# Optimization experiments

Hardware: AMD Instinct MI355X
Metric: run time of the kernel (lower is better)

Reference implementation:

```python
import jax, jax.numpy as jnp
import numpy as np

NX = 64
NY = 64
PATCH_HW = 3          # half-width -> 6x6 patches
P = 2 * PATCH_HW
SIGMA = 0.92
I0 = 1.0 * 1000.0 * 1.0   # eta * N0 * texp


def setup_inputs() -> dict:
    key = jax.random.key(0)
    B, NSPOTS = 8192, 64
    # spot centers uniform over the grid (matches sample(): mu + eps*std + nx/2)
    z = jax.random.uniform(key, (B, 2 * NSPOTS), dtype=jnp.float32,
                           minval=0.0, maxval=float(NX))
    return {"z": z}


def _lam(t, t0, sigma):
    # 0.5 * (erf((t+0.5-t0)/alpha) - erf((t-0.5-t0)/alpha)), alpha = sqrt(2)*sigma
    alpha = jnp.sqrt(jnp.float32(2.0)) * sigma
    return 0.5 * (jax.lax.erf((t + 0.5 - t0) / alpha)
                  - jax.lax.erf((t - 0.5 - t0) / alpha))


def reference(z):
    B = z.shape[0]
    nspots = z.shape[1] // 2
    z = z.reshape(B, 2, nspots)
    x0 = z[:, 0, :]                      # [B, S]
    y0 = z[:, 1, :]                      # [B, S]

    # integer patch origin (torch .round().int() -> round half to even, like jnp.round)
    px = jnp.round(x0).astype(jnp.int32) - PATCH_HW   # [B, S]
    py = jnp.round(y0).astype(jnp.int32) - PATCH_HW
    valid = (px >= 0) & (px < NX - P) & (py >= 0) & (py < NY - P)

    # spot center in patch-local coordinates
    x0p = x0 - px.astype(jnp.float32)    # [B, S]
    y0p = y0 - py.astype(jnp.float32)

    coords = jnp.arange(P, dtype=jnp.float32)                # [P]
    lx = _lam(coords[None, None, :], x0p[..., None], SIGMA)  # [B, S, P]
    ly = _lam(coords[None, None, :], y0p[..., None], SIGMA)  # [B, S, P]
    # outer product: patch[b,s,i,j] = I0 * lx[b,s,i] * ly[b,s,j]  (ij meshgrid)
    patch = I0 * lx[..., :, None] * ly[..., None, :]          # [B, S, P, P]
    patch = jnp.where(valid[..., None, None], patch, 0.0)

    # scatter-add into the [B, NX, NY] grid via flat indices
    pxs = jnp.where(valid, px, 0)
    pys = jnp.where(valid, py, 0)
    rows = pxs[..., None] + jnp.arange(P)                     # [B, S, P]
    cols = pys[..., None] + jnp.arange(P)                     # [B, S, P]
    flat = (jnp.arange(B, dtype=jnp.int32)[:, None, None, None] * (NX * NY)
            + rows[..., :, None] * NY + cols[..., None, :])   # [B, S, P, P]

    mu = jnp.zeros((B * NX * NY,), jnp.float32)
    mu = mu.at[flat.reshape(-1)].add(patch.reshape(-1))
    return mu.reshape(B, 1, NX, NY)
```

## Files before the change

### kernel.cpp

```cpp
#include <hip/hip_runtime.h>


constexpr int NXc = 64;
constexpr int NYc = 64;
constexpr int PATCH_HW = 3;
constexpr int PP = 6;
constexpr float I0c = 1000.0f;
constexpr float INV_ALPHA = 0.76859415f;

__global__ __launch_bounds__(256) void loc_spots_kernel(
        const float* __restrict__ z, float* __restrict__ out) {
    __shared__ float mu[NXc * NYc];
    const int b   = blockIdx.x;
    const int tid = threadIdx.x;

    float4* mu4 = reinterpret_cast<float4*>(mu);
#pragma unroll
    for (int i = 0; i < 4; ++i)
        mu4[tid + i * 256] = make_float4(0.f, 0.f, 0.f, 0.f);
    __syncthreads();

    const int s = tid & 63;
    const int g = tid >> 6;

    const float x0 = z[b * 128 + s];
    const float y0 = z[b * 128 + 64 + s];

    const int px = (int)rintf(x0) - PATCH_HW;
    const int py = (int)rintf(y0) - PATCH_HW;
    const bool valid = (px >= 0) && (px < NXc - PP) && (py >= 0) && (py < NYc - PP);

    if (valid) {
        const float x0p = x0 - (float)px;
        const float y0p = y0 - (float)py;

        float bx[PP + 1], by[PP + 1];
#pragma unroll
        for (int k = 0; k <= PP; ++k) {
            bx[k] = erff(((float)k - 0.5f - x0p) * INV_ALPHA);
            by[k] = erff(((float)k - 0.5f - y0p) * INV_ALPHA);
        }
        float lx[PP], ly[PP];
#pragma unroll
        for (int t = 0; t < PP; ++t) {
            lx[t] = 0.5f * (bx[t + 1] - bx[t]);
            ly[t] = 0.5f * (by[t + 1] - by[t]);
        }

        const int base = px * NYc + py;
#pragma unroll
        for (int q = 0; q < 9; ++q) {
            const int p = g * 9 + q;
            const int i = p / 6;
            const int j = p - i * 6;
            atomicAdd(&mu[base + i * NYc + j], I0c * lx[i] * ly[j]);
        }
    }
    __syncthreads();

    float4* out4 = reinterpret_cast<float4*>(out + (size_t)b * (NXc * NYc));
#pragma unroll
    for (int i = 0; i < 4; ++i)
        out4[tid + i * 256] = mu4[tid + i * 256];
}

extern "C" void kernel_launch(void* const* d_in, const int* in_sizes, int n_in,
                              void* d_out, int out_size, void* d_ws, size_t ws_size,
                              hipStream_t stream) {
    const float* z = (const float*)d_in[0];
    float* out = (float*)d_out;
    const int B = in_sizes[0] / 128;
    loc_spots_kernel<<<B, 256, 0, stream>>>(z, out);
}
```

Before: 201.9 us.

## Use one wave per image with fast erf approximation

Shrinks each block from 256 threads to a single 64-lane wave, so each lane now does all 36 shared-memory atomic adds for its spot. The four waves no longer each recompute the erf values, and the block barriers now cover only one wave. It also swaps erff for an Abramowitz-Stegun polynomial with a fast reciprocal and exp, and folds I0 into lx. The approximation costs some accuracy (about 1e-7 absolute error, times 1000 after scaling), and with fewer threads per block each wave does 16 float4 stores to global memory.

```diff
diff --git a/kernel.cpp b/kernel.cpp
--- a/kernel.cpp
+++ b/kernel.cpp
@@ -3,28 +3,39 @@
 
 constexpr int NXc = 64;
 constexpr int NYc = 64;
+constexpr int IMG = NXc * NYc;
 constexpr int PATCH_HW = 3;
 constexpr int PP = 6;
 constexpr float I0c = 1000.0f;
 constexpr float INV_ALPHA = 0.76859415f;
 
-__global__ __launch_bounds__(256) void loc_spots_kernel(
+__device__ __forceinline__ float fast_erf(float x) {
+    const float ax = __builtin_fabsf(x);
+    const float t  = __builtin_amdgcn_rcpf(__builtin_fmaf(0.3275911f, ax, 1.0f));
+    float y = __builtin_fmaf(1.061405429f, t, -1.453152027f);
+    y = __builtin_fmaf(y, t, 1.421413741f);
+    y = __builtin_fmaf(y, t, -0.284496736f);
+    y = __builtin_fmaf(y, t, 0.254829592f);
+    y = y * t;
+    const float e = __expf(-ax * ax);
+    const float r = __builtin_fmaf(-y, e, 1.0f);
+    return __builtin_copysignf(r, x);
+}
+
+__global__ __launch_bounds__(64) void loc_spots_kernel(
         const float* __restrict__ z, float* __restrict__ out) {
-    __shared__ float mu[NXc * NYc];
-    const int b   = blockIdx.x;
-    const int tid = threadIdx.x;
+    __shared__ float mu[IMG];
+    const int b = blockIdx.x;
+    const int l = threadIdx.x;
+
+    const float x0 = z[b * 128 + l];
+    const float y0 = z[b * 128 + 64 + l];
 
     float4* mu4 = reinterpret_cast<float4*>(mu);
 #pragma unroll
-    for (int i = 0; i < 4; ++i)
-        mu4[tid + i * 256] = make_float4(0.f, 0.f, 0.f, 0.f);
+    for (int i = 0; i < 16; ++i)
+        mu4[l + i * 64] = make_float4(0.f, 0.f, 0.f, 0.f);
     __syncthreads();
-
-    const int s = tid & 63;
-    const int g = tid >> 6;
-
-    const float x0 = z[b * 128 + s];
-    const float y0 = z[b * 128 + 64 + s];
 
     const int px = (int)rintf(x0) - PATCH_HW;
     const int py = (int)rintf(y0) - PATCH_HW;
@@ -37,31 +48,29 @@
         float bx[PP + 1], by[PP + 1];
 #pragma unroll
         for (int k = 0; k <= PP; ++k) {
-            bx[k] = erff(((float)k - 0.5f - x0p) * INV_ALPHA);
-            by[k] = erff(((float)k - 0.5f - y0p) * INV_ALPHA);
+            bx[k] = fast_erf(((float)k - 0.5f - x0p) * INV_ALPHA);
+            by[k] = fast_erf(((float)k - 0.5f - y0p) * INV_ALPHA);
         }
-        float lx[PP], ly[PP];
+        float lxs[PP], ly[PP];
 #pragma unroll
         for (int t = 0; t < PP; ++t) {
-            lx[t] = 0.5f * (bx[t + 1] - bx[t]);
-            ly[t] = 0.5f * (by[t + 1] - by[t]);
+            lxs[t] = (0.5f * I0c) * (bx[t + 1] - bx[t]);
+            ly[t]  = 0.5f * (by[t + 1] - by[t]);
         }
 
         const int base = px * NYc + py;
 #pragma unroll
-        for (int q = 0; q < 9; ++q) {
-            const int p = g * 9 + q;
-            const int i = p / 6;
-            const int j = p - i * 6;
-            atomicAdd(&mu[base + i * NYc + j], I0c * lx[i] * ly[j]);
-        }
+        for (int i = 0; i < PP; ++i)
+#pragma unroll
+            for (int j = 0; j < PP; ++j)
+                atomicAdd(&mu[base + i * NYc + j], lxs[i] * ly[j]);
     }
     __syncthreads();
 
-    float4* out4 = reinterpret_cast<float4*>(out + (size_t)b * (NXc * NYc));
+    float4* out4 = reinterpret_cast<float4*>(out + (size_t)b * IMG);
 #pragma unroll
-    for (int i = 0; i < 4; ++i)
-        out4[tid + i * 256] = mu4[tid + i * 256];
+    for (int i = 0; i < 16; ++i)
+        out4[l + i * 64] = mu4[l + i * 64];
 }
 
 extern "C" void kernel_launch(void* const* d_in, const int* in_sizes, int n_in,
@@ -70,5 +79,5 @@
     const float* z = (const float*)d_in[0];
     float* out = (float*)d_out;
     const int B = in_sizes[0] / 128;
-    loc_spots_kernel<<<B, 256, 0, stream>>>(z, out);
+    loc_spots_kernel<<<B, 64, 0, stream>>>(z, out);
 }
```

Result: faster. 196.1 us (-2.9%).
